# Optimization experiments

Measured on AMD Instinct MI355X. Metric: run time of the kernel, lower is better.

Reference implementation:

```python
import jax, jax.numpy as jnp
import numpy as np
from jax import lax

IMG_SIZE = 512
STRIDE = 16
NUM_ANCHORS = 5
NUM_CLASSES = 80
TOPK = 1000
CONF_THRESH = 0.05
NMS_THRESH = 0.6
ANCHOR_SIZE = [[32, 32], [64, 64], [128, 96], [96, 128], [256, 256]]
B = 32
FMP = IMG_SIZE // STRIDE          # 32
M = FMP * FMP * NUM_ANCHORS       # 5120


def _make_anchors():
    # mirrors YOWO.generate_anchors: grid xy (in pixels) + per-cell anchor wh
    ys, xs = jnp.meshgrid(jnp.arange(FMP), jnp.arange(FMP), indexing='ij')
    xy = jnp.stack([xs, ys], axis=-1).astype(jnp.float32).reshape(-1, 2)   # [HW,2]
    xy = jnp.repeat(xy[:, None, :], NUM_ANCHORS, axis=1) * STRIDE          # [HW,A,2]
    wh = jnp.broadcast_to(jnp.asarray(ANCHOR_SIZE, jnp.float32)[None],
                          (FMP * FMP, NUM_ANCHORS, 2))                     # [HW,A,2]
    return jnp.concatenate([xy, wh], axis=-1).reshape(-1, 4)               # [M,4]


def setup_inputs() -> dict:
    key = jax.random.key(0)
    k1, k2, k3 = jax.random.split(key, 3)
    return {
        'conf_pred': jax.random.normal(k1, (B, M, 1), jnp.float32),
        'cls_pred': jax.random.normal(k2, (B, M, NUM_CLASSES), jnp.float32),
        'reg_pred': jax.random.normal(k3, (B, M, 4), jnp.float32),
        'anchor_boxes': _make_anchors(),
    }


def _decode_bbox(anchors, reg_pred):
    # anchors/reg_pred: [..., 4] -> xyxy boxes in pixels
    xy = jax.nn.sigmoid(reg_pred[..., :2]) * STRIDE + anchors[..., :2]
    wh = jnp.exp(reg_pred[..., 2:]) * anchors[..., 2:]
    return jnp.concatenate([xy - 0.5 * wh, xy + 0.5 * wh], axis=-1)


def _pairwise_iou(boxes):
    # boxes: [K,4] xyxy -> [K,K] IoU with the exact epsilons of YOWO.nms
    x1, y1, x2, y2 = boxes[:, 0], boxes[:, 1], boxes[:, 2], boxes[:, 3]
    areas = (x2 - x1) * (y2 - y1)
    xx1 = jnp.maximum(x1[:, None], x1[None, :])
    yy1 = jnp.maximum(y1[:, None], y1[None, :])
    xx2 = jnp.minimum(x2[:, None], x2[None, :])
    yy2 = jnp.minimum(y2[:, None], y2[None, :])
    w = jnp.maximum(1e-28, xx2 - xx1)
    h = jnp.maximum(1e-28, yy2 - yy1)
    inter = w * h
    return inter / (areas[:, None] + areas[None, :] - inter + 1e-14)


def _sequential_nms_keep(iou):
    # boxes assumed sorted by descending score; greedy sequential suppression
    K = iou.shape[0]
    idx = jnp.arange(K)

    def body(i, keep):
        sup = (iou[i] > NMS_THRESH) & (idx > i) & keep[i]
        return keep & ~sup

    return lax.fori_loop(0, K, body, jnp.ones(K, bool))


def reference(conf_pred, cls_pred, reg_pred, anchor_boxes):
    # scoring: sigmoid(obj) * softmax(cls), max over classes  -> [B,M]
    score_all = jax.nn.sigmoid(conf_pred) * jax.nn.softmax(cls_pred, axis=-1)
    scores = jnp.max(score_all, axis=-1)
    labels = jnp.argmax(score_all, axis=-1)

    # topk (lax.top_k returns scores sorted descending)  -> [B,TOPK]
    scores, idx = lax.top_k(scores, TOPK)
    labels = jnp.take_along_axis(labels, idx, axis=1)
    reg_sel = jnp.take_along_axis(reg_pred, idx[..., None], axis=1)
    anc_sel = anchor_boxes[idx]                                   # [B,TOPK,4]

    bboxes = jnp.clip(_decode_bbox(anc_sel, reg_sel) / IMG_SIZE, 0.0, 1.0)

    # per-class NMS via class-offset trick (boxes in [0,1], offset 2.0 per class)
    boxes_off = bboxes + 2.0 * labels.astype(bboxes.dtype)[..., None]
    iou = jax.vmap(_pairwise_iou)(boxes_off)                      # [B,TOPK,TOPK]
    nms_keep = jax.vmap(_sequential_nms_keep)(iou)                # [B,TOPK] bool

    keep = nms_keep & (scores >= CONF_THRESH)
    scores_out = jnp.where(keep, scores, 0.0)
    return scores_out, labels, bboxes, keep
```

## Files before the change

kernel.cpp:

```cpp
#include <hip/hip_runtime.h>
#include <cstdint>
#include <math.h>


constexpr int B = 32;
constexpr int M = 5120;
constexpr int C = 80;
constexpr int K = 1000;

constexpr int OFF_SCORE = 0;
constexpr int OFF_LAB   = B * K;
constexpr int OFF_BOX   = 2 * B * K;
constexpr int OFF_KEEP  = 2 * B * K + 4 * B * K;

constexpr size_t WS_KEYS     = 0;
constexpr size_t WS_LABELS   = WS_KEYS   + (size_t)B * M * 8;
constexpr size_t WS_SELSC    = WS_LABELS + (size_t)B * M * 4;
constexpr size_t WS_BOXOFF   = WS_SELSC + (size_t)B * K * 4;
constexpr size_t WS_MASK     = WS_BOXOFF + (size_t)B * K * 4 * 4;

__device__ __forceinline__ double exp_fast(double t) {
    constexpr double INVLN2 = 1.4426950408889634074;
    constexpr double LN2HI  = 6.93147180369123816490e-01;
    constexpr double LN2LO  = 1.90821492927058770002e-10;
    double kd = rint(t * INVLN2);
    kd = fmin(fmax(kd, -1000.0), 1000.0);
    int k = (int)kd;
    double r = (t - kd * LN2HI) - kd * LN2LO;
    constexpr double C3 = 1.0/6.0,        C4  = 1.0/24.0,        C5  = 1.0/120.0;
    constexpr double C6 = 1.0/720.0,      C7  = 1.0/5040.0,      C8  = 1.0/40320.0;
    constexpr double C9 = 1.0/362880.0,   C10 = 1.0/3628800.0,   C11 = 1.0/39916800.0;
    constexpr double C12 = 1.0/479001600.0, C13 = 1.0/6227020800.0;
    double s = fma(r, C13, C12);
    s = fma(r, s, C11); s = fma(r, s, C10); s = fma(r, s, C9);
    s = fma(r, s, C8);  s = fma(r, s, C7);  s = fma(r, s, C6);
    s = fma(r, s, C5);  s = fma(r, s, C4);  s = fma(r, s, C3);
    double u = r * r;
    double q = fma(r, s, 0.5);
    double v = fma(u, q, r);
    double p = 1.0 + v;
    long long sbits = (long long)(1023 + k) << 52;
    return p * __longlong_as_double(sbits);
}
__device__ __forceinline__ float expf_cr(float x) {
    return (float)exp_fast((double)x);
}
__device__ __forceinline__ float sigm_np(float x) {
    float e = expf_cr(-x);
    return __fdiv_rn(1.0f, __fadd_rn(1.0f, e));
}

__global__ void __launch_bounds__(256)
k_scores(const float* __restrict__ conf, const float* __restrict__ cls,
         unsigned long long* __restrict__ keys, int* __restrict__ labels) {
    int b = blockIdx.y;
    int g0 = blockIdx.x * 32;
    int tid = threadIdx.x;
    __shared__ float s_lds[32];
    if (tid < 32) {
        s_lds[tid] = sigm_np(conf[(size_t)b * M + g0 + tid]);
    }
    __syncthreads();
    int grp = tid >> 3;
    int j   = tid & 7;
    int m = g0 + grp;
    size_t base = ((size_t)b * M + m) * C + j;
    float x[10];
#pragma unroll
    for (int k = 0; k < 10; k++) x[k] = cls[base + 8 * k];
    float mx = x[0];
#pragma unroll
    for (int k = 1; k < 10; k++) mx = fmaxf(mx, x[k]);
#pragma unroll
    for (int d = 1; d < 8; d <<= 1) mx = fmaxf(mx, __shfl_xor(mx, d, 64));
    float e[10];
#pragma unroll
    for (int k = 0; k < 10; k++) e[k] = expf_cr(__fsub_rn(x[k], mx));
    float r = e[0];
#pragma unroll
    for (int k = 1; k < 10; k++) r = __fadd_rn(r, e[k]);
    float t1  = __fadd_rn(r,  __shfl_xor(r, 1, 64));
    float t2  = __fadd_rn(t1, __shfl_xor(t1, 2, 64));
    float sum = __fadd_rn(t2, __shfl_xor(t2, 4, 64));
    float s = s_lds[grp];
    float best = -1.0f; int bc = 0;
#pragma unroll
    for (int k = 0; k < 10; k++) {
        float q = __fdiv_rn(e[k], sum);
        float p = __fmul_rn(s, q);
        if (p > best) { best = p; bc = 8 * k + j; }
    }
#pragma unroll
    for (int d = 1; d < 8; d <<= 1) {
        float op = __shfl_xor(best, d, 64);
        int   oc = __shfl_xor(bc,   d, 64);
        if (op > best || (op == best && oc < bc)) { best = op; bc = oc; }
    }
    if (j == 0) {
        keys[(size_t)b * M + m] =
            ((unsigned long long)__float_as_uint(best) << 32) |
            (unsigned long long)(0xFFFFFFFFu - (unsigned)m);
        labels[(size_t)b * M + m] = bc;
    }
}

__device__ __forceinline__ void decode_write(
    int b, int rank, int m, float score, int lab,
    const float* __restrict__ reg, const float* __restrict__ anchors,
    float* __restrict__ out, float4* __restrict__ boxes_off,
    float* __restrict__ sel_score)
{
    float4 r = ((const float4*)reg)[(size_t)b * M + m];
    float4 a = ((const float4*)anchors)[m];
    float cx = __fadd_rn(__fmul_rn(sigm_np(r.x), 16.0f), a.x);
    float cy = __fadd_rn(__fmul_rn(sigm_np(r.y), 16.0f), a.y);
    float w  = __fmul_rn(expf_cr(r.z), a.z);
    float h  = __fmul_rn(expf_cr(r.w), a.w);
    float x1 = __fdiv_rn(__fsub_rn(cx, __fmul_rn(0.5f, w)), 512.0f);
    float y1 = __fdiv_rn(__fsub_rn(cy, __fmul_rn(0.5f, h)), 512.0f);
    float x2 = __fdiv_rn(__fadd_rn(cx, __fmul_rn(0.5f, w)), 512.0f);
    float y2 = __fdiv_rn(__fadd_rn(cy, __fmul_rn(0.5f, h)), 512.0f);
    x1 = fminf(fmaxf(x1, 0.0f), 1.0f);
    y1 = fminf(fmaxf(y1, 0.0f), 1.0f);
    x2 = fminf(fmaxf(x2, 0.0f), 1.0f);
    y2 = fminf(fmaxf(y2, 0.0f), 1.0f);
    ((float4*)(out + OFF_BOX))[b * K + rank] = make_float4(x1, y1, x2, y2);
    out[OFF_LAB + b * K + rank] = (float)lab;
    float off = __fmul_rn(2.0f, (float)lab);
    boxes_off[b * K + rank] = make_float4(__fadd_rn(x1, off), __fadd_rn(y1, off),
                                          __fadd_rn(x2, off), __fadd_rn(y2, off));
    sel_score[b * K + rank] = score;
}

__device__ __forceinline__ void cx_reg(unsigned long long& v, int i, int jsz, int ksz) {
    unsigned long long vp = __shfl_xor(v, jsz, 64);
    bool takeMax = (((i & ksz) == 0) == ((i & jsz) == 0));
    v = takeMax ? (vp > v ? vp : v) : (vp < v ? vp : v);
}

__global__ void __launch_bounds__(1024)
k_topk(const unsigned long long* __restrict__ keys,
       const int* __restrict__ labels,
       const float* __restrict__ reg, const float* __restrict__ anchors,
       float* __restrict__ out, float4* __restrict__ boxes_off,
       float* __restrict__ sel_score) {
    int b = blockIdx.x;
    int tid = threadIdx.x;
    int lane = tid & 63;
    int wv   = tid >> 6;
    const unsigned long long* kb = keys + (size_t)b * M;

    __shared__ unsigned int hist[2048];
    __shared__ unsigned long long cand[2048];
    __shared__ unsigned int waveSuf[17];
    __shared__ int scnt, thrBin, ovf;

    for (int i = tid; i < 2048; i += 1024) hist[i] = 0;
    if (tid == 0) { scnt = 0; ovf = 0; }
    __syncthreads();

    unsigned long long k5[5];
#pragma unroll
    for (int i = 0; i < 5; i++) {
        k5[i] = kb[tid + i * 1024];
        atomicAdd(&hist[(unsigned)(k5[i] >> 51)], 1u);
    }
    __syncthreads();

    unsigned h0 = hist[2 * tid], h1 = hist[2 * tid + 1];
    unsigned pr = h0 + h1;
    unsigned s = pr;
#pragma unroll
    for (int d = 1; d < 64; d <<= 1) {
        unsigned o = __shfl_down(s, d, 64);
        if (lane + d < 64) s += o;
    }
    if (lane == 0) waveSuf[wv] = s;
    if (tid == 0) waveSuf[16] = 0;
    __syncthreads();
    if (wv == 0) {
        unsigned t = (lane < 16) ? waveSuf[lane] : 0u;
#pragma unroll
        for (int d = 1; d < 16; d <<= 1) {
            unsigned o = __shfl_down(t, d, 64);
            if (lane + d < 64) t += o;
        }
        if (lane < 16) waveSuf[lane] = t;
    }
    __syncthreads();
    {
        unsigned aboveWave = waveSuf[wv + 1];
        unsigned aboveLane = s - pr;
        unsigned suf1 = aboveWave + aboveLane + h1;
        unsigned suf0 = suf1 + h0;
        if (suf0 >= (unsigned)K && suf0 - h0 < (unsigned)K) thrBin = 2 * tid;
        if (suf1 >= (unsigned)K && suf1 - h1 < (unsigned)K) thrBin = 2 * tid + 1;
    }
    __syncthreads();
    int T = thrBin;
#pragma unroll
    for (int i = 0; i < 5; i++) {
        if ((int)(k5[i] >> 51) >= T) {
            int pos = atomicAdd(&scnt, 1);
            if (pos < 2048) cand[pos] = k5[i]; else ovf = 1;
        }
    }
    __syncthreads();
    if (!ovf) {
        int S = scnt;
        int N = (S <= 1024) ? 1024 : 2048;
        for (int i = tid; i < 2048; i += 1024)
            if (i >= S) cand[i] = 0ull;
        __syncthreads();
        bool act = (128 * wv < N);
        int i0 = 128 * wv + lane, i1 = i0 + 64;
        unsigned long long v0 = 0ull, v1 = 0ull;
        if (act) { v0 = cand[i0]; v1 = cand[i1]; }
        if (act) {
#pragma unroll
            for (int ksz = 2; ksz <= 64; ksz <<= 1)
#pragma unroll
                for (int jsz = ksz >> 1; jsz > 0; jsz >>= 1) {
                    cx_reg(v0, i0, jsz, ksz);
                    cx_reg(v1, i1, jsz, ksz);
                }
            cand[i0] = v0; cand[i1] = v1;
        }
        __syncthreads();
        for (int ksz = 128; ksz <= N; ksz <<= 1) {
            for (int jsz = ksz >> 1; jsz >= 64; jsz >>= 1) {
                if (tid < (N >> 1)) {
                    int i = 2 * tid - (tid & (jsz - 1));
                    unsigned long long a = cand[i], c = cand[i + jsz];
                    bool desc = ((i & ksz) == 0);
                    if ((a < c) == desc) { cand[i] = c; cand[i + jsz] = a; }
                }
                __syncthreads();
            }
            if (act) {
                v0 = cand[i0]; v1 = cand[i1];
#pragma unroll
                for (int jsz = 32; jsz > 0; jsz >>= 1) {
                    cx_reg(v0, i0, jsz, ksz);
                    cx_reg(v1, i1, jsz, ksz);
                }
                cand[i0] = v0; cand[i1] = v1;
            }
            __syncthreads();
        }
        if (tid < K) {
            unsigned long long key = cand[tid];
            int mm = (int)(0xFFFFFFFFu - (unsigned)(key & 0xFFFFFFFFu));
            float sc = __uint_as_float((unsigned)(key >> 32));
            int lab = labels[(size_t)b * M + mm];
            decode_write(b, tid, mm, sc, lab, reg, anchors, out, boxes_off, sel_score);
        }
    } else {
#pragma unroll
        for (int i = 0; i < 5; i++) {
            unsigned long long my = k5[i];
            int rank = 0;
            for (int j = 0; j < M; j++) rank += (kb[j] > my) ? 1 : 0;
            if (rank < K) {
                int mm = tid + i * 1024;
                float sc = __uint_as_float((unsigned)(my >> 32));
                int lab = labels[(size_t)b * M + mm];
                decode_write(b, rank, mm, sc, lab, reg, anchors, out, boxes_off, sel_score);
            }
        }
    }
}

__global__ void __launch_bounds__(256)
k_mask(const float4* __restrict__ boxes_off,
       unsigned long long* __restrict__ mask) {
    int b    = blockIdx.y;
    int wv   = threadIdx.x >> 6;
    int lane = threadIdx.x & 63;
    int p = blockIdx.x * 4 + wv;
    int r = (int)((sqrtf((float)(8 * p + 1)) - 1.0f) * 0.5f);
    int tri = (r * (r + 1)) >> 1;
    if (tri > p)          { r -= 1; tri = (r * (r + 1)) >> 1; }
    else if (p - tri > r) { r += 1; tri = (r * (r + 1)) >> 1; }
    int W = p - tri;

    __shared__ float4 sj[4][64];
    __shared__ float  sa[4][64];
    int j = W * 64 + lane;
    float4 bx = (j < K) ? boxes_off[b * K + j]
                        : make_float4(3e30f, 3e30f, -3e30f, -3e30f);
    sj[wv][lane] = bx;
    sa[wv][lane] = __fmul_rn(__fsub_rn(bx.z, bx.x), __fsub_rn(bx.w, bx.y));
    int i = r * 64 + lane;
    bool rowOk = (i < K);
    float4 bi = make_float4(0.f, 0.f, 0.f, 0.f);
    float ai = 0.f;
    if (rowOk) {
        bi = boxes_off[b * K + i];
        ai = __fmul_rn(__fsub_rn(bi.z, bi.x), __fsub_rn(bi.w, bi.y));
    }
    __syncthreads();
    if (!rowOk) return;
    constexpr double MID = (double)0.6f + 0x1.0p-25;
    unsigned long long bits = 0ull;
#pragma unroll 8
    for (int jj = 0; jj < 64; jj++) {
        float4 bj = sj[wv][jj];
        float aj = sa[wv][jj];
        float xx1 = fmaxf(bi.x, bj.x), yy1 = fmaxf(bi.y, bj.y);
        float xx2 = fminf(bi.z, bj.z), yy2 = fminf(bi.w, bj.w);
        float ww = fmaxf(1e-28f, __fsub_rn(xx2, xx1));
        float hh = fmaxf(1e-28f, __fsub_rn(yy2, yy1));
        float inter = __fmul_rn(ww, hh);
        float denom = __fadd_rn(__fsub_rn(__fadd_rn(ai, aj), inter), 1e-14f);
        if ((double)inter > MID * (double)denom) bits |= (1ull << jj);
    }
    mask[((size_t)b * K + i) * 16 + W] = bits;
}

__global__ void __launch_bounds__(1024)
k_nms(const unsigned long long* __restrict__ mask,
      const float* __restrict__ sel_score,
      float* __restrict__ out) {
    int b = blockIdx.x;
    int j = threadIdx.x;
    int w = j >> 6;
    int jb = j & 63;
    __shared__ unsigned long long U[16], L[16];
    __shared__ int flag[2];
    unsigned long long rw[16];
    if (j < K) {
        const ulonglong2* rp2 =
            (const ulonglong2*)(mask + ((size_t)b * K + j) * 16);
#pragma unroll
        for (int t = 0; t < 8; t++) {
            ulonglong2 v = rp2[t];
            rw[2 * t] = v.x; rw[2 * t + 1] = v.y;
        }
#pragma unroll
        for (int t = 0; t < 16; t++) {
            unsigned long long bm =
                (t < w) ? ~0ull
                        : ((t == w && jb != 0) ? ((1ull << jb) - 1ull) : 0ull);
            rw[t] &= bm;
        }
    } else {
#pragma unroll
        for (int t = 0; t < 16; t++) rw[t] = 0ull;
    }
    if (j < 16) { U[j] = (j < 15) ? ~0ull : ((1ull << 40) - 1); L[j] = 0ull; }
    if (j == 0) { flag[0] = 0; flag[1] = 0; }
    __syncthreads();
    for (int k = 0; k < 1025; k++) {
        unsigned long long supU = 0ull, supL = 0ull;
#pragma unroll
        for (int t = 0; t < 16; t++) {
            unsigned long long Ut = U[t], Lt = L[t];
            supU |= Lt & rw[t];
            supL |= Ut & rw[t];
        }
        bool nu = (j < K) && (supU == 0ull);
        bool nl = (j < K) && (supL == 0ull);
        __syncthreads();
        unsigned long long bu = __ballot(nu);
        unsigned long long bl = __ballot(nl);
        if (jb == 0) {
            U[w] = bu; L[w] = bl;
            if (bu != bl) flag[k & 1] = 1;
        }
        if (j == 0) flag[(k + 1) & 1] = 0;
        __syncthreads();
        if (flag[k & 1] == 0) break;
    }
    if (j < K) {
        bool kp = ((U[w] >> jb) & 1ull) != 0ull;
        float s = sel_score[b * K + j];
        kp = kp && (s >= 0.05f);
        out[OFF_SCORE + b * K + j] = kp ? s : 0.0f;
        out[OFF_KEEP + b * K + j]  = kp ? 1.0f : 0.0f;
    }
}

extern "C" void kernel_launch(void* const* d_in, const int* in_sizes, int n_in,
                              void* d_out, int out_size, void* d_ws, size_t ws_size,
                              hipStream_t stream) {
    const float* conf    = (const float*)d_in[0];
    const float* cls     = (const float*)d_in[1];
    const float* reg     = (const float*)d_in[2];
    const float* anchors = (const float*)d_in[3];
    float* out = (float*)d_out;
    char* ws = (char*)d_ws;

    unsigned long long* keys = (unsigned long long*)(ws + WS_KEYS);
    int*    labels   = (int*)(ws + WS_LABELS);
    float*  sel_sc   = (float*)(ws + WS_SELSC);
    float4* boxes_off = (float4*)(ws + WS_BOXOFF);
    unsigned long long* mask = (unsigned long long*)(ws + WS_MASK);

    k_scores<<<dim3(160, B), 256, 0, stream>>>(conf, cls, keys, labels);
    k_topk  <<<B, 1024, 0, stream>>>(keys, labels, reg, anchors, out, boxes_off, sel_sc);
    k_mask  <<<dim3(34, B), 256, 0, stream>>>(boxes_off, mask);
    k_nms   <<<32, 1024, 0, stream>>>(mask, sel_sc, out);
}
```

Baseline: 146.9 us.

## Refine top-k radix threshold to fit 1024 candidates and defer box decode

Adds a second 11-bit radix histogram pass when the threshold bin would overflow 1024 candidates, so the bitonic sort always runs on 1024 keys held in registers, one per thread, instead of up to 2048 keys swapped through shared memory. Box decoding leaves the single-block-per-batch top-k kernel. It is recomputed from the sorted keys in the mask kernel and again in the NMS kernel, which also writes the output boxes. The intermediate offset-box and score buffers are removed. The cost is redundant sigmoid/exp decode work in the mask kernel, where each box is decoded many times across blocks, plus an extra histogram pass in some batches.

```diff
diff --git a/kernel.cpp b/kernel.cpp
--- a/kernel.cpp
+++ b/kernel.cpp
@@ -13,11 +13,10 @@
 constexpr int OFF_BOX   = 2 * B * K;
 constexpr int OFF_KEEP  = 2 * B * K + 4 * B * K;
 
-constexpr size_t WS_KEYS     = 0;
-constexpr size_t WS_LABELS   = WS_KEYS   + (size_t)B * M * 8;
-constexpr size_t WS_SELSC    = WS_LABELS + (size_t)B * M * 4;
-constexpr size_t WS_BOXOFF   = WS_SELSC + (size_t)B * K * 4;
-constexpr size_t WS_MASK     = WS_BOXOFF + (size_t)B * K * 4 * 4;
+constexpr size_t WS_KEYS   = 0;
+constexpr size_t WS_LABELS = WS_KEYS   + (size_t)B * M * 8;
+constexpr size_t WS_SKEYS  = WS_LABELS + (size_t)B * M * 4;
+constexpr size_t WS_MASK   = WS_SKEYS  + (size_t)B * K * 8;
 
 __device__ __forceinline__ double exp_fast(double t) {
     constexpr double INVLN2 = 1.4426950408889634074;
@@ -50,66 +49,8 @@
     return __fdiv_rn(1.0f, __fadd_rn(1.0f, e));
 }
 
-__global__ void __launch_bounds__(256)
-k_scores(const float* __restrict__ conf, const float* __restrict__ cls,
-         unsigned long long* __restrict__ keys, int* __restrict__ labels) {
-    int b = blockIdx.y;
-    int g0 = blockIdx.x * 32;
-    int tid = threadIdx.x;
-    __shared__ float s_lds[32];
-    if (tid < 32) {
-        s_lds[tid] = sigm_np(conf[(size_t)b * M + g0 + tid]);
-    }
-    __syncthreads();
-    int grp = tid >> 3;
-    int j   = tid & 7;
-    int m = g0 + grp;
-    size_t base = ((size_t)b * M + m) * C + j;
-    float x[10];
-#pragma unroll
-    for (int k = 0; k < 10; k++) x[k] = cls[base + 8 * k];
-    float mx = x[0];
-#pragma unroll
-    for (int k = 1; k < 10; k++) mx = fmaxf(mx, x[k]);
-#pragma unroll
-    for (int d = 1; d < 8; d <<= 1) mx = fmaxf(mx, __shfl_xor(mx, d, 64));
-    float e[10];
-#pragma unroll
-    for (int k = 0; k < 10; k++) e[k] = expf_cr(__fsub_rn(x[k], mx));
-    float r = e[0];
-#pragma unroll
-    for (int k = 1; k < 10; k++) r = __fadd_rn(r, e[k]);
-    float t1  = __fadd_rn(r,  __shfl_xor(r, 1, 64));
-    float t2  = __fadd_rn(t1, __shfl_xor(t1, 2, 64));
-    float sum = __fadd_rn(t2, __shfl_xor(t2, 4, 64));
-    float s = s_lds[grp];
-    float best = -1.0f; int bc = 0;
-#pragma unroll
-    for (int k = 0; k < 10; k++) {
-        float q = __fdiv_rn(e[k], sum);
-        float p = __fmul_rn(s, q);
-        if (p > best) { best = p; bc = 8 * k + j; }
-    }
-#pragma unroll
-    for (int d = 1; d < 8; d <<= 1) {
-        float op = __shfl_xor(best, d, 64);
-        int   oc = __shfl_xor(bc,   d, 64);
-        if (op > best || (op == best && oc < bc)) { best = op; bc = oc; }
-    }
-    if (j == 0) {
-        keys[(size_t)b * M + m] =
-            ((unsigned long long)__float_as_uint(best) << 32) |
-            (unsigned long long)(0xFFFFFFFFu - (unsigned)m);
-        labels[(size_t)b * M + m] = bc;
-    }
-}
-
-__device__ __forceinline__ void decode_write(
-    int b, int rank, int m, float score, int lab,
-    const float* __restrict__ reg, const float* __restrict__ anchors,
-    float* __restrict__ out, float4* __restrict__ boxes_off,
-    float* __restrict__ sel_score)
-{
+__device__ __forceinline__ float4 decode_box(
+    int b, int m, const float* __restrict__ reg, const float* __restrict__ anchors) {
     float4 r = ((const float4*)reg)[(size_t)b * M + m];
     float4 a = ((const float4*)anchors)[m];
     float cx = __fadd_rn(__fmul_rn(sigm_np(r.x), 16.0f), a.x);
@@ -124,12 +65,61 @@
     y1 = fminf(fmaxf(y1, 0.0f), 1.0f);
     x2 = fminf(fmaxf(x2, 0.0f), 1.0f);
     y2 = fminf(fmaxf(y2, 0.0f), 1.0f);
-    ((float4*)(out + OFF_BOX))[b * K + rank] = make_float4(x1, y1, x2, y2);
-    out[OFF_LAB + b * K + rank] = (float)lab;
-    float off = __fmul_rn(2.0f, (float)lab);
-    boxes_off[b * K + rank] = make_float4(__fadd_rn(x1, off), __fadd_rn(y1, off),
-                                          __fadd_rn(x2, off), __fadd_rn(y2, off));
-    sel_score[b * K + rank] = score;
+    return make_float4(x1, y1, x2, y2);
+}
+
+__global__ void __launch_bounds__(256)
+k_scores(const float* __restrict__ conf, const float* __restrict__ cls,
+         unsigned long long* __restrict__ keys, int* __restrict__ labels) {
+    int b = blockIdx.y;
+    int g0 = blockIdx.x * 32;
+    int tid = threadIdx.x;
+    __shared__ float s_lds[32];
+    if (tid < 32) {
+        s_lds[tid] = sigm_np(conf[(size_t)b * M + g0 + tid]);
+    }
+    __syncthreads();
+    int grp = tid >> 3;
+    int j   = tid & 7;
+    int m = g0 + grp;
+    size_t base = ((size_t)b * M + m) * C + j;
+    float x[10];
+#pragma unroll
+    for (int k = 0; k < 10; k++) x[k] = cls[base + 8 * k];
+    float mx = x[0];
+#pragma unroll
+    for (int k = 1; k < 10; k++) mx = fmaxf(mx, x[k]);
+#pragma unroll
+    for (int d = 1; d < 8; d <<= 1) mx = fmaxf(mx, __shfl_xor(mx, d, 64));
+    float e[10];
+#pragma unroll
+    for (int k = 0; k < 10; k++) e[k] = expf_cr(__fsub_rn(x[k], mx));
+    float r = e[0];
+#pragma unroll
+    for (int k = 1; k < 10; k++) r = __fadd_rn(r, e[k]);
+    float t1  = __fadd_rn(r,  __shfl_xor(r, 1, 64));
+    float t2  = __fadd_rn(t1, __shfl_xor(t1, 2, 64));
+    float sum = __fadd_rn(t2, __shfl_xor(t2, 4, 64));
+    float s = s_lds[grp];
+    float best = -1.0f; int bc = 0;
+#pragma unroll
+    for (int k = 0; k < 10; k++) {
+        float q = __fdiv_rn(e[k], sum);
+        float p = __fmul_rn(s, q);
+        if (p > best) { best = p; bc = 8 * k + j; }
+    }
+#pragma unroll
+    for (int d = 1; d < 8; d <<= 1) {
+        float op = __shfl_xor(best, d, 64);
+        int   oc = __shfl_xor(bc,   d, 64);
+        if (op > best || (op == best && oc < bc)) { best = op; bc = oc; }
+    }
+    if (j == 0) {
+        keys[(size_t)b * M + m] =
+            ((unsigned long long)__float_as_uint(best) << 32) |
+            (unsigned long long)(0xFFFFFFFFu - (unsigned)m);
+        labels[(size_t)b * M + m] = bc;
+    }
 }
 
 __device__ __forceinline__ void cx_reg(unsigned long long& v, int i, int jsz, int ksz) {
@@ -141,9 +131,8 @@
 __global__ void __launch_bounds__(1024)
 k_topk(const unsigned long long* __restrict__ keys,
        const int* __restrict__ labels,
-       const float* __restrict__ reg, const float* __restrict__ anchors,
-       float* __restrict__ out, float4* __restrict__ boxes_off,
-       float* __restrict__ sel_score) {
+       unsigned long long* __restrict__ skeys,
+       float* __restrict__ out) {
     int b = blockIdx.x;
     int tid = threadIdx.x;
     int lane = tid & 63;
@@ -151,9 +140,9 @@
     const unsigned long long* kb = keys + (size_t)b * M;
 
     __shared__ unsigned int hist[2048];
-    __shared__ unsigned long long cand[2048];
+    __shared__ unsigned long long cand[1024];
     __shared__ unsigned int waveSuf[17];
-    __shared__ int scnt, thrBin, ovf;
+    __shared__ int scnt, thrBin, thrBin2, sA, sH, sS2, ovf;
 
     for (int i = tid; i < 2048; i += 1024) hist[i] = 0;
     if (tid == 0) { scnt = 0; ovf = 0; }
@@ -167,93 +156,124 @@
     }
     __syncthreads();
 
-    unsigned h0 = hist[2 * tid], h1 = hist[2 * tid + 1];
-    unsigned pr = h0 + h1;
-    unsigned s = pr;
-#pragma unroll
-    for (int d = 1; d < 64; d <<= 1) {
-        unsigned o = __shfl_down(s, d, 64);
-        if (lane + d < 64) s += o;
-    }
-    if (lane == 0) waveSuf[wv] = s;
-    if (tid == 0) waveSuf[16] = 0;
-    __syncthreads();
-    if (wv == 0) {
-        unsigned t = (lane < 16) ? waveSuf[lane] : 0u;
-#pragma unroll
-        for (int d = 1; d < 16; d <<= 1) {
-            unsigned o = __shfl_down(t, d, 64);
-            if (lane + d < 64) t += o;
-        }
-        if (lane < 16) waveSuf[lane] = t;
-    }
-    __syncthreads();
     {
+        unsigned h0 = hist[2 * tid], h1 = hist[2 * tid + 1];
+        unsigned pr = h0 + h1;
+        unsigned s = pr;
+#pragma unroll
+        for (int d = 1; d < 64; d <<= 1) {
+            unsigned o = __shfl_down(s, d, 64);
+            if (lane + d < 64) s += o;
+        }
+        if (lane == 0) waveSuf[wv] = s;
+        if (tid == 0) waveSuf[16] = 0;
+        __syncthreads();
+        if (wv == 0) {
+            unsigned t = (lane < 16) ? waveSuf[lane] : 0u;
+#pragma unroll
+            for (int d = 1; d < 16; d <<= 1) {
+                unsigned o = __shfl_down(t, d, 64);
+                if (lane + d < 64) t += o;
+            }
+            if (lane < 16) waveSuf[lane] = t;
+        }
+        __syncthreads();
         unsigned aboveWave = waveSuf[wv + 1];
         unsigned aboveLane = s - pr;
         unsigned suf1 = aboveWave + aboveLane + h1;
         unsigned suf0 = suf1 + h0;
-        if (suf0 >= (unsigned)K && suf0 - h0 < (unsigned)K) thrBin = 2 * tid;
-        if (suf1 >= (unsigned)K && suf1 - h1 < (unsigned)K) thrBin = 2 * tid + 1;
-    }
-    __syncthreads();
-    int T = thrBin;
+        if (suf0 >= (unsigned)K && suf0 - h0 < (unsigned)K) {
+            thrBin = 2 * tid; sA = (int)(suf0 - h0); sH = (int)h0;
+        }
+        if (suf1 >= (unsigned)K && suf1 - h1 < (unsigned)K) {
+            thrBin = 2 * tid + 1; sA = (int)(suf1 - h1); sH = (int)h1;
+        }
+    }
+    __syncthreads();
+    int T1 = thrBin, A = sA, H = sH;
+    bool refined = (A + H > 1024);
+    int T2 = 0;
+
+    if (refined) {
+        for (int i = tid; i < 2048; i += 1024) hist[i] = 0;
+        __syncthreads();
+#pragma unroll
+        for (int i = 0; i < 5; i++)
+            if ((int)(k5[i] >> 51) == T1)
+                atomicAdd(&hist[(unsigned)((k5[i] >> 40) & 2047)], 1u);
+        __syncthreads();
+        unsigned KK = (unsigned)(K - A);
+        unsigned g0 = hist[2 * tid], g1 = hist[2 * tid + 1];
+        unsigned pr = g0 + g1;
+        unsigned s = pr;
+#pragma unroll
+        for (int d = 1; d < 64; d <<= 1) {
+            unsigned o = __shfl_down(s, d, 64);
+            if (lane + d < 64) s += o;
+        }
+        if (lane == 0) waveSuf[wv] = s;
+        if (tid == 0) waveSuf[16] = 0;
+        __syncthreads();
+        if (wv == 0) {
+            unsigned t = (lane < 16) ? waveSuf[lane] : 0u;
+#pragma unroll
+            for (int d = 1; d < 16; d <<= 1) {
+                unsigned o = __shfl_down(t, d, 64);
+                if (lane + d < 64) t += o;
+            }
+            if (lane < 16) waveSuf[lane] = t;
+        }
+        __syncthreads();
+        unsigned aboveWave = waveSuf[wv + 1];
+        unsigned aboveLane = s - pr;
+        unsigned suf1 = aboveWave + aboveLane + g1;
+        unsigned suf0 = suf1 + g0;
+        if (suf0 >= KK && suf0 - g0 < KK) { thrBin2 = 2 * tid;     sS2 = A + (int)suf0; }
+        if (suf1 >= KK && suf1 - g1 < KK) { thrBin2 = 2 * tid + 1; sS2 = A + (int)suf1; }
+        __syncthreads();
+        T2 = thrBin2;
+    }
+
 #pragma unroll
     for (int i = 0; i < 5; i++) {
-        if ((int)(k5[i] >> 51) >= T) {
+        int bin = (int)(k5[i] >> 51);
+        bool sel = refined
+                 ? (bin > T1 || (bin == T1 && (int)((k5[i] >> 40) & 2047) >= T2))
+                 : (bin >= T1);
+        if (sel) {
             int pos = atomicAdd(&scnt, 1);
-            if (pos < 2048) cand[pos] = k5[i]; else ovf = 1;
-        }
-    }
-    __syncthreads();
+            if (pos < 1024) cand[pos] = k5[i]; else ovf = 1;
+        }
+    }
+    __syncthreads();
+
     if (!ovf) {
         int S = scnt;
-        int N = (S <= 1024) ? 1024 : 2048;
-        for (int i = tid; i < 2048; i += 1024)
-            if (i >= S) cand[i] = 0ull;
-        __syncthreads();
-        bool act = (128 * wv < N);
-        int i0 = 128 * wv + lane, i1 = i0 + 64;
-        unsigned long long v0 = 0ull, v1 = 0ull;
-        if (act) { v0 = cand[i0]; v1 = cand[i1]; }
-        if (act) {
-#pragma unroll
-            for (int ksz = 2; ksz <= 64; ksz <<= 1)
-#pragma unroll
-                for (int jsz = ksz >> 1; jsz > 0; jsz >>= 1) {
-                    cx_reg(v0, i0, jsz, ksz);
-                    cx_reg(v1, i1, jsz, ksz);
-                }
-            cand[i0] = v0; cand[i1] = v1;
-        }
-        __syncthreads();
-        for (int ksz = 128; ksz <= N; ksz <<= 1) {
+        if (tid >= S) cand[tid] = 0ull;
+        __syncthreads();
+        unsigned long long v = cand[tid];
+#pragma unroll
+        for (int ksz = 2; ksz <= 64; ksz <<= 1)
+#pragma unroll
+            for (int jsz = ksz >> 1; jsz > 0; jsz >>= 1)
+                cx_reg(v, tid, jsz, ksz);
+        for (int ksz = 128; ksz <= 1024; ksz <<= 1) {
             for (int jsz = ksz >> 1; jsz >= 64; jsz >>= 1) {
-                if (tid < (N >> 1)) {
-                    int i = 2 * tid - (tid & (jsz - 1));
-                    unsigned long long a = cand[i], c = cand[i + jsz];
-                    bool desc = ((i & ksz) == 0);
-                    if ((a < c) == desc) { cand[i] = c; cand[i + jsz] = a; }
-                }
+                cand[tid] = v;
+                __syncthreads();
+                unsigned long long vp = cand[tid ^ jsz];
+                bool takeMax = (((tid & ksz) == 0) == ((tid & jsz) == 0));
+                v = takeMax ? (vp > v ? vp : v) : (vp < v ? vp : v);
                 __syncthreads();
             }
-            if (act) {
-                v0 = cand[i0]; v1 = cand[i1];
-#pragma unroll
-                for (int jsz = 32; jsz > 0; jsz >>= 1) {
-                    cx_reg(v0, i0, jsz, ksz);
-                    cx_reg(v1, i1, jsz, ksz);
-                }
-                cand[i0] = v0; cand[i1] = v1;
-            }
-            __syncthreads();
+#pragma unroll
+            for (int jsz = 32; jsz > 0; jsz >>= 1)
+                cx_reg(v, tid, jsz, ksz);
         }
         if (tid < K) {
-            unsigned long long key = cand[tid];
-            int mm = (int)(0xFFFFFFFFu - (unsigned)(key & 0xFFFFFFFFu));
-            float sc = __uint_as_float((unsigned)(key >> 32));
-            int lab = labels[(size_t)b * M + mm];
-            decode_write(b, tid, mm, sc, lab, reg, anchors, out, boxes_off, sel_score);
+            int mm = (int)(0xFFFFFFFFu - (unsigned)(v & 0xFFFFFFFFu));
+            skeys[(size_t)b * K + tid] = v;
+            out[OFF_LAB + b * K + tid] = (float)labels[(size_t)b * M + mm];
         }
     } else {
 #pragma unroll
@@ -263,16 +283,17 @@
             for (int j = 0; j < M; j++) rank += (kb[j] > my) ? 1 : 0;
             if (rank < K) {
                 int mm = tid + i * 1024;
-                float sc = __uint_as_float((unsigned)(my >> 32));
-                int lab = labels[(size_t)b * M + mm];
-                decode_write(b, rank, mm, sc, lab, reg, anchors, out, boxes_off, sel_score);
+                skeys[(size_t)b * K + rank] = my;
+                out[OFF_LAB + b * K + rank] = (float)labels[(size_t)b * M + mm];
             }
         }
     }
 }
 
 __global__ void __launch_bounds__(256)
-k_mask(const float4* __restrict__ boxes_off,
+k_mask(const unsigned long long* __restrict__ skeys,
+       const int* __restrict__ labels,
+       const float* __restrict__ reg, const float* __restrict__ anchors,
        unsigned long long* __restrict__ mask) {
     int b    = blockIdx.y;
     int wv   = threadIdx.x >> 6;
@@ -287,16 +308,28 @@
     __shared__ float4 sj[4][64];
     __shared__ float  sa[4][64];
     int j = W * 64 + lane;
-    float4 bx = (j < K) ? boxes_off[b * K + j]
-                        : make_float4(3e30f, 3e30f, -3e30f, -3e30f);
-    sj[wv][lane] = bx;
-    sa[wv][lane] = __fmul_rn(__fsub_rn(bx.z, bx.x), __fsub_rn(bx.w, bx.y));
+    float4 bj = make_float4(3e30f, 3e30f, -3e30f, -3e30f);
+    if (j < K) {
+        unsigned long long sk = skeys[(size_t)b * K + j];
+        int m = (int)(0xFFFFFFFFu - (unsigned)(sk & 0xFFFFFFFFu));
+        float off = __fmul_rn(2.0f, (float)labels[(size_t)b * M + m]);
+        float4 bb = decode_box(b, m, reg, anchors);
+        bj = make_float4(__fadd_rn(bb.x, off), __fadd_rn(bb.y, off),
+                         __fadd_rn(bb.z, off), __fadd_rn(bb.w, off));
+    }
+    sj[wv][lane] = bj;
+    sa[wv][lane] = __fmul_rn(__fsub_rn(bj.z, bj.x), __fsub_rn(bj.w, bj.y));
     int i = r * 64 + lane;
     bool rowOk = (i < K);
     float4 bi = make_float4(0.f, 0.f, 0.f, 0.f);
     float ai = 0.f;
     if (rowOk) {
-        bi = boxes_off[b * K + i];
+        unsigned long long sk = skeys[(size_t)b * K + i];
+        int m = (int)(0xFFFFFFFFu - (unsigned)(sk & 0xFFFFFFFFu));
+        float off = __fmul_rn(2.0f, (float)labels[(size_t)b * M + m]);
+        float4 bb = decode_box(b, m, reg, anchors);
+        bi = make_float4(__fadd_rn(bb.x, off), __fadd_rn(bb.y, off),
+                         __fadd_rn(bb.z, off), __fadd_rn(bb.w, off));
         ai = __fmul_rn(__fsub_rn(bi.z, bi.x), __fsub_rn(bi.w, bi.y));
     }
     __syncthreads();
@@ -305,10 +338,10 @@
     unsigned long long bits = 0ull;
 #pragma unroll 8
     for (int jj = 0; jj < 64; jj++) {
-        float4 bj = sj[wv][jj];
+        float4 bj2 = sj[wv][jj];
         float aj = sa[wv][jj];
-        float xx1 = fmaxf(bi.x, bj.x), yy1 = fmaxf(bi.y, bj.y);
-        float xx2 = fminf(bi.z, bj.z), yy2 = fminf(bi.w, bj.w);
+        float xx1 = fmaxf(bi.x, bj2.x), yy1 = fmaxf(bi.y, bj2.y);
+        float xx2 = fminf(bi.z, bj2.z), yy2 = fminf(bi.w, bj2.w);
         float ww = fmaxf(1e-28f, __fsub_rn(xx2, xx1));
         float hh = fmaxf(1e-28f, __fsub_rn(yy2, yy1));
         float inter = __fmul_rn(ww, hh);
@@ -320,7 +353,8 @@
 
 __global__ void __launch_bounds__(1024)
 k_nms(const unsigned long long* __restrict__ mask,
-      const float* __restrict__ sel_score,
+      const unsigned long long* __restrict__ skeys,
+      const float* __restrict__ reg, const float* __restrict__ anchors,
       float* __restrict__ out) {
     int b = blockIdx.x;
     int j = threadIdx.x;
@@ -329,7 +363,13 @@
     __shared__ unsigned long long U[16], L[16];
     __shared__ int flag[2];
     unsigned long long rw[16];
+    float s = 0.0f;
+    float4 bb = make_float4(0.f, 0.f, 0.f, 0.f);
     if (j < K) {
+        unsigned long long sk = skeys[(size_t)b * K + j];
+        s = __uint_as_float((unsigned)(sk >> 32));
+        int m = (int)(0xFFFFFFFFu - (unsigned)(sk & 0xFFFFFFFFu));
+        bb = decode_box(b, m, reg, anchors);
         const ulonglong2* rp2 =
             (const ulonglong2*)(mask + ((size_t)b * K + j) * 16);
 #pragma unroll
@@ -374,8 +414,8 @@
     }
     if (j < K) {
         bool kp = ((U[w] >> jb) & 1ull) != 0ull;
-        float s = sel_score[b * K + j];
         kp = kp && (s >= 0.05f);
+        ((float4*)(out + OFF_BOX))[b * K + j] = bb;
         out[OFF_SCORE + b * K + j] = kp ? s : 0.0f;
         out[OFF_KEEP + b * K + j]  = kp ? 1.0f : 0.0f;
     }
@@ -391,14 +431,13 @@
     float* out = (float*)d_out;
     char* ws = (char*)d_ws;
 
-    unsigned long long* keys = (unsigned long long*)(ws + WS_KEYS);
-    int*    labels   = (int*)(ws + WS_LABELS);
-    float*  sel_sc   = (float*)(ws + WS_SELSC);
-    float4* boxes_off = (float4*)(ws + WS_BOXOFF);
-    unsigned long long* mask = (unsigned long long*)(ws + WS_MASK);
+    unsigned long long* keys  = (unsigned long long*)(ws + WS_KEYS);
+    int*                labels = (int*)(ws + WS_LABELS);
+    unsigned long long* skeys = (unsigned long long*)(ws + WS_SKEYS);
+    unsigned long long* mask  = (unsigned long long*)(ws + WS_MASK);
 
     k_scores<<<dim3(160, B), 256, 0, stream>>>(conf, cls, keys, labels);
-    k_topk  <<<B, 1024, 0, stream>>>(keys, labels, reg, anchors, out, boxes_off, sel_sc);
-    k_mask  <<<dim3(34, B), 256, 0, stream>>>(boxes_off, mask);
-    k_nms   <<<32, 1024, 0, stream>>>(mask, sel_sc, out);
-}
+    k_topk  <<<B, 1024, 0, stream>>>(keys, labels, skeys, out);
+    k_mask  <<<dim3(34, B), 256, 0, stream>>>(skeys, labels, reg, anchors, mask);
+    k_nms   <<<32, 1024, 0, stream>>>(mask, skeys, reg, anchors, out);
+}
```

Measured after the change: 150.3 us. 1.02x slower.

## Add second radix-histogram pass to cap top-k candidates at 1024 and sort in registers

Applied to the files above, without the earlier changes.

The top-k kernel now checks whether the first 11-bit radix bin leaves more than 1024 candidates. If so, it runs a second histogram over the next 11 key bits within the threshold bin to tighten the cutoff. With at most 1024 candidates, the bitonic sort keeps one element per thread in registers and uses shared memory only for the cross-wave exchange steps, which removes the old 2048-element two-per-thread path. The cost is an extra histogram and scan pass with several block barriers whenever refinement triggers.

```diff
diff --git a/kernel.cpp b/kernel.cpp
--- a/kernel.cpp
+++ b/kernel.cpp
@@ -151,9 +151,9 @@
     const unsigned long long* kb = keys + (size_t)b * M;
 
     __shared__ unsigned int hist[2048];
-    __shared__ unsigned long long cand[2048];
+    __shared__ unsigned long long cand[1024];
     __shared__ unsigned int waveSuf[17];
-    __shared__ int scnt, thrBin, ovf;
+    __shared__ int scnt, thrBin, thrBin2, sA, ovf;
 
     for (int i = tid; i < 2048; i += 1024) hist[i] = 0;
     if (tid == 0) { scnt = 0; ovf = 0; }
@@ -167,91 +167,128 @@
     }
     __syncthreads();
 
-    unsigned h0 = hist[2 * tid], h1 = hist[2 * tid + 1];
-    unsigned pr = h0 + h1;
-    unsigned s = pr;
-#pragma unroll
-    for (int d = 1; d < 64; d <<= 1) {
-        unsigned o = __shfl_down(s, d, 64);
-        if (lane + d < 64) s += o;
-    }
-    if (lane == 0) waveSuf[wv] = s;
-    if (tid == 0) waveSuf[16] = 0;
-    __syncthreads();
-    if (wv == 0) {
-        unsigned t = (lane < 16) ? waveSuf[lane] : 0u;
-#pragma unroll
-        for (int d = 1; d < 16; d <<= 1) {
-            unsigned o = __shfl_down(t, d, 64);
-            if (lane + d < 64) t += o;
-        }
-        if (lane < 16) waveSuf[lane] = t;
-    }
-    __syncthreads();
     {
+        unsigned h0 = hist[2 * tid], h1 = hist[2 * tid + 1];
+        unsigned pr = h0 + h1;
+        unsigned s = pr;
+#pragma unroll
+        for (int d = 1; d < 64; d <<= 1) {
+            unsigned o = __shfl_down(s, d, 64);
+            if (lane + d < 64) s += o;
+        }
+        if (lane == 0) waveSuf[wv] = s;
+        if (tid == 0) waveSuf[16] = 0;
+        __syncthreads();
+        if (wv == 0) {
+            unsigned t = (lane < 16) ? waveSuf[lane] : 0u;
+#pragma unroll
+            for (int d = 1; d < 16; d <<= 1) {
+                unsigned o = __shfl_down(t, d, 64);
+                if (lane + d < 64) t += o;
+            }
+            if (lane < 16) waveSuf[lane] = t;
+        }
+        __syncthreads();
         unsigned aboveWave = waveSuf[wv + 1];
         unsigned aboveLane = s - pr;
         unsigned suf1 = aboveWave + aboveLane + h1;
         unsigned suf0 = suf1 + h0;
-        if (suf0 >= (unsigned)K && suf0 - h0 < (unsigned)K) thrBin = 2 * tid;
-        if (suf1 >= (unsigned)K && suf1 - h1 < (unsigned)K) thrBin = 2 * tid + 1;
-    }
-    __syncthreads();
-    int T = thrBin;
+        if (suf0 >= (unsigned)K && suf0 - h0 < (unsigned)K) {
+            thrBin = 2 * tid; sA = (int)(suf0 - h0);
+        }
+        if (suf1 >= (unsigned)K && suf1 - h1 < (unsigned)K) {
+            thrBin = 2 * tid + 1; sA = (int)(suf1 - h1);
+        }
+    }
+    __syncthreads();
+    int T1 = thrBin, A = sA;
+    unsigned S1 = 0;
+    {
+        S1 = (unsigned)A + hist[T1];
+    }
+    bool refined = (S1 > 1024u);
+    int T2 = 0;
+
+    if (refined) {
+        __syncthreads();
+        for (int i = tid; i < 2048; i += 1024) hist[i] = 0;
+        __syncthreads();
+#pragma unroll
+        for (int i = 0; i < 5; i++)
+            if ((int)(k5[i] >> 51) == T1)
+                atomicAdd(&hist[(unsigned)((k5[i] >> 40) & 2047)], 1u);
+        __syncthreads();
+        unsigned KK = (unsigned)(K - A);
+        unsigned g0 = hist[2 * tid], g1 = hist[2 * tid + 1];
+        unsigned pr = g0 + g1;
+        unsigned s = pr;
+#pragma unroll
+        for (int d = 1; d < 64; d <<= 1) {
+            unsigned o = __shfl_down(s, d, 64);
+            if (lane + d < 64) s += o;
+        }
+        if (lane == 0) waveSuf[wv] = s;
+        if (tid == 0) waveSuf[16] = 0;
+        __syncthreads();
+        if (wv == 0) {
+            unsigned t = (lane < 16) ? waveSuf[lane] : 0u;
+#pragma unroll
+            for (int d = 1; d < 16; d <<= 1) {
+                unsigned o = __shfl_down(t, d, 64);
+                if (lane + d < 64) t += o;
+            }
+            if (lane < 16) waveSuf[lane] = t;
+        }
+        __syncthreads();
+        unsigned aboveWave = waveSuf[wv + 1];
+        unsigned aboveLane = s - pr;
+        unsigned suf1 = aboveWave + aboveLane + g1;
+        unsigned suf0 = suf1 + g0;
+        if (suf0 >= KK && suf0 - g0 < KK) thrBin2 = 2 * tid;
+        if (suf1 >= KK && suf1 - g1 < KK) thrBin2 = 2 * tid + 1;
+        __syncthreads();
+        T2 = thrBin2;
+    }
+
 #pragma unroll
     for (int i = 0; i < 5; i++) {
-        if ((int)(k5[i] >> 51) >= T) {
+        int bin = (int)(k5[i] >> 51);
+        bool sel = refined
+                 ? (bin > T1 || (bin == T1 && (int)((k5[i] >> 40) & 2047) >= T2))
+                 : (bin >= T1);
+        if (sel) {
             int pos = atomicAdd(&scnt, 1);
-            if (pos < 2048) cand[pos] = k5[i]; else ovf = 1;
-        }
-    }
-    __syncthreads();
+            if (pos < 1024) cand[pos] = k5[i]; else ovf = 1;
+        }
+    }
+    __syncthreads();
+
     if (!ovf) {
         int S = scnt;
-        int N = (S <= 1024) ? 1024 : 2048;
-        for (int i = tid; i < 2048; i += 1024)
-            if (i >= S) cand[i] = 0ull;
-        __syncthreads();
-        bool act = (128 * wv < N);
-        int i0 = 128 * wv + lane, i1 = i0 + 64;
-        unsigned long long v0 = 0ull, v1 = 0ull;
-        if (act) { v0 = cand[i0]; v1 = cand[i1]; }
-        if (act) {
-#pragma unroll
-            for (int ksz = 2; ksz <= 64; ksz <<= 1)
-#pragma unroll
-                for (int jsz = ksz >> 1; jsz > 0; jsz >>= 1) {
-                    cx_reg(v0, i0, jsz, ksz);
-                    cx_reg(v1, i1, jsz, ksz);
-                }
-            cand[i0] = v0; cand[i1] = v1;
-        }
-        __syncthreads();
-        for (int ksz = 128; ksz <= N; ksz <<= 1) {
+        if (tid >= S) cand[tid] = 0ull;
+        __syncthreads();
+        unsigned long long v = cand[tid];
+#pragma unroll
+        for (int ksz = 2; ksz <= 64; ksz <<= 1)
+#pragma unroll
+            for (int jsz = ksz >> 1; jsz > 0; jsz >>= 1)
+                cx_reg(v, tid, jsz, ksz);
+        for (int ksz = 128; ksz <= 1024; ksz <<= 1) {
             for (int jsz = ksz >> 1; jsz >= 64; jsz >>= 1) {
-                if (tid < (N >> 1)) {
-                    int i = 2 * tid - (tid & (jsz - 1));
-                    unsigned long long a = cand[i], c = cand[i + jsz];
-                    bool desc = ((i & ksz) == 0);
-                    if ((a < c) == desc) { cand[i] = c; cand[i + jsz] = a; }
-                }
+                cand[tid] = v;
+                __syncthreads();
+                unsigned long long vp = cand[tid ^ jsz];
+                bool takeMax = (((tid & ksz) == 0) == ((tid & jsz) == 0));
+                v = takeMax ? (vp > v ? vp : v) : (vp < v ? vp : v);
                 __syncthreads();
             }
-            if (act) {
-                v0 = cand[i0]; v1 = cand[i1];
-#pragma unroll
-                for (int jsz = 32; jsz > 0; jsz >>= 1) {
-                    cx_reg(v0, i0, jsz, ksz);
-                    cx_reg(v1, i1, jsz, ksz);
-                }
-                cand[i0] = v0; cand[i1] = v1;
-            }
-            __syncthreads();
+#pragma unroll
+            for (int jsz = 32; jsz > 0; jsz >>= 1)
+                cx_reg(v, tid, jsz, ksz);
         }
         if (tid < K) {
-            unsigned long long key = cand[tid];
-            int mm = (int)(0xFFFFFFFFu - (unsigned)(key & 0xFFFFFFFFu));
-            float sc = __uint_as_float((unsigned)(key >> 32));
+            int mm = (int)(0xFFFFFFFFu - (unsigned)(v & 0xFFFFFFFFu));
+            float sc = __uint_as_float((unsigned)(v >> 32));
             int lab = labels[(size_t)b * M + mm];
             decode_write(b, tid, mm, sc, lab, reg, anchors, out, boxes_off, sel_score);
         }
```

Measured after the change: 139.5 us. -5.0%, faster.
